# Optimization experiments

Measured on AMD Instinct MI355X. Metric: run time of the kernel, lower is better.

## Reference

```python
import jax, jax.numpy as jnp
import numpy as np

B, N, D_MODEL = 8, 1024, 512
H, DK = 8, 64
STATIONS = 128
MASK_NEG = -1e9
LN_EPS = 1e-6


def setup_inputs() -> dict:
    key = jax.random.key(0)
    ks = jax.random.split(key, 9)
    return {
        "hidden_states": jax.random.normal(ks[0], (B, N, D_MODEL), dtype=jnp.float32),
        "rpe": jax.random.normal(ks[1], (B, H, N, N), dtype=jnp.float32) * 0.1,
        "Wq": jax.random.normal(ks[2], (H * DK, D_MODEL), dtype=jnp.float32) * 0.02,
        "Wk": jax.random.normal(ks[3], (H * DK, D_MODEL), dtype=jnp.float32) * 0.02,
        "Wv": jax.random.normal(ks[4], (H * DK, D_MODEL), dtype=jnp.float32) * 0.02,
        "fc_w": jax.random.normal(ks[5], (D_MODEL, H * DK), dtype=jnp.float32) * 0.02,
        "fc_b": jnp.zeros((D_MODEL,), dtype=jnp.float32),
        "ln_g": jnp.ones((D_MODEL,), dtype=jnp.float32),
        "ln_b": jnp.zeros((D_MODEL,), dtype=jnp.float32),
    }


def _star_mask(n, stations):
    # q_k_mask: query i attends to key j iff j < stations or i == j
    idx = jnp.arange(n)
    return (idx[None, :] < stations) | (idx[:, None] == idx[None, :])  # [n, n] bool


def reference(hidden_states, rpe, Wq, Wk, Wv, fc_w, fc_b, ln_g, ln_b):
    b, n, _ = hidden_states.shape
    residual = hidden_states
    q = (hidden_states @ Wq.T).reshape(b, n, H, DK)
    k = (hidden_states @ Wk.T).reshape(b, n, H, DK)
    v = (hidden_states @ Wv.T).reshape(b, n, H, DK)
    # sparse star+self-loop QK^T with inline RPE add (dense emulation of QKP_mm_tvm)
    scores = jnp.einsum("bihd,bjhd->bhij", q, k) + rpe  # [b,h,n,n]
    mask = _star_mask(n, STATIONS)
    scores = jnp.where(mask[None, None], scores, MASK_NEG)
    scores = scores / jnp.sqrt(jnp.float32(DK))
    attn = jax.nn.softmax(scores, axis=-1)
    # AttnV_mm_tvm: sparse attn-weights times V
    ctx = jnp.einsum("bhij,bjhd->bihd", attn, v).reshape(b, n, H * DK)
    ctx = ctx @ fc_w.T + fc_b + residual
    mu = jnp.mean(ctx, axis=-1, keepdims=True)
    var = jnp.var(ctx, axis=-1, keepdims=True)
    return (ctx - mu) / jnp.sqrt(var + LN_EPS) * ln_g + ln_b
```

## Files before the change

### kernel.cpp

```cpp
#include <hip/hip_runtime.h>
#include <hip/hip_bf16.h>
#include <math.h>

#define B_  8
#define N_  1024
#define DM  512
#define H_  8
#define DK_ 64
#define ST  128

typedef __attribute__((ext_vector_type(8))) short short8;
typedef __attribute__((ext_vector_type(4))) float floatx4;

#define GLD16(gp, lp)                                                          \
    __builtin_amdgcn_global_load_lds(                                          \
        (const __attribute__((address_space(1))) void*)(gp),                   \
        (__attribute__((address_space(3))) void*)(lp), 16, 0, 0)

__device__ __forceinline__ float b2f(short u) {
    union { unsigned int i; float f; } c;
    c.i = ((unsigned int)(unsigned short)u) << 16;
    return c.f;
}
__device__ __forceinline__ unsigned short f2b(float f) {
    __hip_bfloat16 t = __float2bfloat16(f);
    return *(unsigned short*)&t;
}

struct CastArgs {
    const float* src[5];
    unsigned short* dst[5];
};

__global__ __launch_bounds__(256)
void cast_bf16_kernel(CastArgs a)
{
    const int bx = blockIdx.x;
    int j, base;
    if (bx < 2048) { j = 0; base = bx; }
    else { const int r = bx - 2048; j = 1 + (r >> 7); base = r & 127; }
    const float* __restrict__ s = a.src[j];
    unsigned short* __restrict__ d = a.dst[j];
    const int i = (base * 256 + threadIdx.x) * 8;
    float4 x0 = *(const float4*)&s[i];
    float4 x1 = *(const float4*)&s[i + 4];
    ushort4 o0, o1;
    o0.x = f2b(x0.x); o0.y = f2b(x0.y); o0.z = f2b(x0.z); o0.w = f2b(x0.w);
    o1.x = f2b(x1.x); o1.y = f2b(x1.y); o1.z = f2b(x1.z); o1.w = f2b(x1.w);
    *(ushort4*)&d[i] = o0;
    *(ushort4*)&d[i + 4] = o1;
}

__device__ __forceinline__
void gemm_step(const unsigned short* Ac, const unsigned short* Bc,
               int wm, int wn, int mrow, int koff, floatx4 acc[4][4])
{
    short8 af[4], bf[4];
    #pragma unroll
    for (int t = 0; t < 4; ++t) {
        af[t] = *(const short8*)&Ac[(wm * 64 + t * 16 + mrow) * 32 + koff];
        bf[t] = *(const short8*)&Bc[(wn * 64 + t * 16 + mrow) * 32 + koff];
    }
    #pragma unroll
    for (int mt = 0; mt < 4; ++mt)
        #pragma unroll
        for (int nt = 0; nt < 4; ++nt)
            acc[mt][nt] = __builtin_amdgcn_mfma_f32_16x16x32_bf16(
                af[mt], bf[nt], acc[mt][nt], 0, 0, 0);
}

__device__ __forceinline__
void gemm_core(const unsigned short* __restrict__ A,
               const unsigned short* __restrict__ W,
               int m0, int n0, unsigned short* As, unsigned short* Bs,
               floatx4 acc[4][4])
{
    const int tid = threadIdx.x;
    const int lane = tid & 63;
    const int wave = tid >> 6;
    const int wm = wave >> 1, wn = wave & 1;
    const int srow = tid >> 2;
    const int skq  = (tid & 3) * 8;
    const unsigned short* Ag = A + (size_t)(m0 + srow) * 512 + skq;
    const unsigned short* Bg = W + (size_t)(n0 + srow) * 512 + skq;
    const int mrow = lane & 15;
    const int koff = (lane >> 4) * 8;

    unsigned short* A0 = As;        unsigned short* A1 = As + 4096;
    unsigned short* B0 = Bs;        unsigned short* B1 = Bs + 4096;

#define STAGE4(Ad, Bd, off)                                                    \
    do {                                                                       \
        GLD16(Ag + (off),            &(Ad)[tid * 8]);                          \
        GLD16(Ag + 64 * 512 + (off), &(Ad)[2048 + tid * 8]);                   \
        GLD16(Bg + (off),            &(Bd)[tid * 8]);                          \
        GLD16(Bg + 64 * 512 + (off), &(Bd)[2048 + tid * 8]);                   \
    } while (0)

    STAGE4(A0, B0, 0);
    __syncthreads();

    #pragma unroll
    for (int kt = 0; kt < 512; kt += 64) {
        STAGE4(A1, B1, kt + 32);
        gemm_step(A0, B0, wm, wn, mrow, koff, acc);
        __syncthreads();
        if (kt + 64 < 512)
            STAGE4(A0, B0, kt + 64);
        gemm_step(A1, B1, wm, wn, mrow, koff, acc);
        __syncthreads();
    }
#undef STAGE4
}

__global__ __launch_bounds__(256)
void qkv_gemm_kernel(const unsigned short* __restrict__ A,
                     const unsigned short* __restrict__ W0,
                     const unsigned short* __restrict__ W1,
                     const unsigned short* __restrict__ W2,
                     unsigned short* __restrict__ qo,
                     unsigned short* __restrict__ ko,
                     unsigned short* __restrict__ vto)
{
    __shared__ __align__(16) unsigned short As[2 * 128 * 32];
    __shared__ __align__(16) unsigned short Bs[2 * 128 * 32];
    const int by = blockIdx.y;
    const int sel = by >> 2;
    const unsigned short* W = (sel == 0) ? W0 : (sel == 1 ? W1 : W2);
    const int m0 = blockIdx.x * 128;
    const int n0 = (by & 3) * 128;

    floatx4 acc[4][4];
    #pragma unroll
    for (int i = 0; i < 4; ++i)
        #pragma unroll
        for (int j = 0; j < 4; ++j)
            acc[i][j] = (floatx4){0.f, 0.f, 0.f, 0.f};

    gemm_core(A, W, m0, n0, As, Bs, acc);

    const int lane = threadIdx.x & 63;
    const int wave = threadIdx.x >> 6;
    const int wm = wave >> 1, wn = wave & 1;
    const int lx = lane & 15;
    const int rq = (lane >> 4) * 4;

    if (sel == 2) {
        #pragma unroll
        for (int mt = 0; mt < 4; ++mt) {
            const int mrow = m0 + wm * 64 + mt * 16 + rq;
            const int bb = mrow >> 10, tok = mrow & 1023;
            #pragma unroll
            for (int nt = 0; nt < 4; ++nt) {
                const int c = n0 + wn * 64 + nt * 16 + lx;
                const int hh = c >> 6, d = c & 63;
                ushort4 pk;
                pk.x = f2b(acc[mt][nt][0]); pk.y = f2b(acc[mt][nt][1]);
                pk.z = f2b(acc[mt][nt][2]); pk.w = f2b(acc[mt][nt][3]);
                *(ushort4*)&vto[((size_t)(bb * H_ + hh) * DK_ + d) * N_ + tok] = pk;
            }
        }
    } else {
        unsigned short* O = (sel == 0) ? qo : ko;
        #pragma unroll
        for (int mt = 0; mt < 4; ++mt) {
            const int mrow = m0 + wm * 64 + mt * 16 + rq;
            const int bb = mrow >> 10, tok = mrow & 1023;
            #pragma unroll
            for (int nt = 0; nt < 4; ++nt) {
                const int c = n0 + wn * 64 + nt * 16 + lx;
                const int hh = c >> 6, d = c & 63;
                unsigned short* p =
                    O + ((size_t)(bb * H_ + hh) * N_ + tok) * DK_ + d;
                #pragma unroll
                for (int r = 0; r < 4; ++r)
                    p[(size_t)r * DK_] = f2b(acc[mt][nt][r]);
            }
        }
    }
}

__global__ __launch_bounds__(256)
void attn_kernel(const unsigned short* __restrict__ qg,
                 const unsigned short* __restrict__ kg,
                 const unsigned short* __restrict__ vtg,
                 const float* __restrict__ rpe,
                 unsigned short* __restrict__ ctx)
{
    __shared__ __align__(16) unsigned short P[64 * 136];
    __shared__ __align__(16) unsigned short Vd[64 * 72];

    const int tid  = threadIdx.x;
    const int lane = tid & 63;
    const int w    = tid >> 6;
    const int lx   = lane & 15;
    const int quad = lane >> 4;
    const int qb = blockIdx.x * 64;
    const int h  = blockIdx.y, b = blockIdx.z;
    const int bh = b * H_ + h;
    const unsigned short* qh  = qg  + (size_t)bh * N_ * DK_;
    const unsigned short* kh  = kg  + (size_t)bh * N_ * DK_;
    const unsigned short* vth = vtg + (size_t)bh * DK_ * N_;
    const float* rp = rpe + ((size_t)bh * N_ + qb) * N_;
    const bool has_self = (qb >= ST);

    if (has_self) {
        const int d = tid >> 2, t16 = (tid & 3) * 16;
        const unsigned short* vs = vth + (size_t)d * N_ + qb + t16;
        *(short8*)&Vd[d * 72 + t16]     = *(const short8*)vs;
        *(short8*)&Vd[d * 72 + t16 + 8] = *(const short8*)(vs + 8);
    }

    float sself = -1e30f;
    if (has_self) {
        const int i = qb + w * 16 + lx;
        const unsigned short* qr = qh + (size_t)i * DK_ + quad * 16;
        const unsigned short* kr = kh + (size_t)i * DK_ + quad * 16;
        short8 q0 = *(const short8*)qr, q1 = *(const short8*)(qr + 8);
        short8 k0 = *(const short8*)kr, k1 = *(const short8*)(kr + 8);
        float dot = 0.f;
        #pragma unroll
        for (int j = 0; j < 8; ++j) {
            dot = fmaf(b2f(q0[j]), b2f(k0[j]), dot);
            dot = fmaf(b2f(q1[j]), b2f(k1[j]), dot);
        }
        dot += __shfl_xor(dot, 16, 64);
        dot += __shfl_xor(dot, 32, 64);
        const float rd = rp[(size_t)(w * 16 + lx) * N_ + (qb + w * 16 + lx)];
        sself = (dot + rd) * 0.125f;
    }

    float rv[4][8];
    {
        const float* rbase = rp + (size_t)(w * 16 + quad * 4) * N_ + lx;
        #pragma unroll
        for (int r = 0; r < 4; ++r)
            #pragma unroll
            for (int nt = 0; nt < 8; ++nt)
                rv[r][nt] = rbase[(size_t)r * N_ + nt * 16];
    }

    short8 aq[2];
    {
        const unsigned short* qrow =
            qh + (size_t)(qb + w * 16 + lx) * DK_ + quad * 8;
        aq[0] = *(const short8*)qrow;
        aq[1] = *(const short8*)(qrow + 32);
    }
    floatx4 sacc[8];
    #pragma unroll
    for (int nt = 0; nt < 8; ++nt) sacc[nt] = (floatx4){0.f, 0.f, 0.f, 0.f};
    #pragma unroll
    for (int nt = 0; nt < 8; ++nt) {
        const unsigned short* krow =
            kh + (size_t)(nt * 16 + lx) * DK_ + quad * 8;
        short8 b0 = *(const short8*)krow;
        short8 b1 = *(const short8*)(krow + 32);
        sacc[nt] = __builtin_amdgcn_mfma_f32_16x16x32_bf16(aq[0], b0, sacc[nt], 0, 0, 0);
        sacc[nt] = __builtin_amdgcn_mfma_f32_16x16x32_bf16(aq[1], b1, sacc[nt], 0, 0, 0);
    }

    float l4[4], ps4[4];
    #pragma unroll
    for (int r = 0; r < 4; ++r) {
        float sv[8];
        float mx = -1e30f;
        #pragma unroll
        for (int nt = 0; nt < 8; ++nt) {
            sv[nt] = (sacc[nt][r] + rv[r][nt]) * 0.125f;
            mx = fmaxf(mx, sv[nt]);
        }
        #pragma unroll
        for (int o = 1; o < 16; o <<= 1)
            mx = fmaxf(mx, __shfl_xor(mx, o, 64));
        const float ss = __shfl(sself, quad * 4 + r, 64);
        mx = fmaxf(mx, ss);
        float sum = 0.f;
        #pragma unroll
        for (int nt = 0; nt < 8; ++nt) {
            sv[nt] = __expf(sv[nt] - mx);
            sum += sv[nt];
        }
// ... 157 lines not shown
                s[mt][r]  += __shfl_xor(s[mt][r],  o, 64);
                ss[mt][r] += __shfl_xor(ss[mt][r], o, 64);
            }
    if (lx == 0) {
        #pragma unroll
        for (int mt = 0; mt < 2; ++mt)
            #pragma unroll
            for (int r = 0; r < 4; ++r) {
                lsum[mt * 16 + quad * 4 + r][wv] = s[mt][r];
                lsq [mt * 16 + quad * 4 + r][wv] = ss[mt][r];
            }
    }
    __syncthreads();

    #pragma unroll
    for (int mt = 0; mt < 2; ++mt)
        #pragma unroll
        for (int r = 0; r < 4; ++r) {
            const int rl = mt * 16 + quad * 4 + r;
            float ts = 0.f, tss = 0.f;
            #pragma unroll
            for (int u = 0; u < 8; ++u) { ts += lsum[rl][u]; tss += lsq[rl][u]; }
            const float mean = ts * (1.0f / DM);
            const float var  = tss * (1.0f / DM) - mean * mean;
            const float rstd = rsqrtf(var + 1e-6f);
            const size_t row = (size_t)(m0 + rl);
            #pragma unroll
            for (int nt = 0; nt < 4; ++nt) {
                const int c = wv * 64 + nt * 16 + lx;
                out[row * 512 + c] =
                    (acc[mt][nt][r] - mean) * rstd * g[c] + bb[c];
            }
        }
}

extern "C" void kernel_launch(void* const* d_in, const int* in_sizes, int n_in,
                              void* d_out, int out_size, void* d_ws, size_t ws_size,
                              hipStream_t stream)
{
    (void)in_sizes; (void)n_in; (void)out_size; (void)ws_size;
    const float* hidden = (const float*)d_in[0];
    const float* rpe    = (const float*)d_in[1];
    const float* Wq     = (const float*)d_in[2];
    const float* Wk     = (const float*)d_in[3];
    const float* Wv     = (const float*)d_in[4];
    const float* fc_w   = (const float*)d_in[5];
    const float* fc_b   = (const float*)d_in[6];
    const float* ln_g   = (const float*)d_in[7];
    const float* ln_b   = (const float*)d_in[8];
    float* out = (float*)d_out;
    char* ws = (char*)d_ws;

    const size_t MB = 1024 * 1024;
    unsigned short* hb  = (unsigned short*)(ws + 0 * MB);
    unsigned short* wq  = (unsigned short*)(ws + 8 * MB);
    unsigned short* wk  = (unsigned short*)(ws + 8 * MB + 512 * 1024);
    unsigned short* wv  = (unsigned short*)(ws + 9 * MB);
    unsigned short* wf  = (unsigned short*)(ws + 9 * MB + 512 * 1024);
    unsigned short* qB  = (unsigned short*)(ws + 16 * MB);
    unsigned short* kB  = (unsigned short*)(ws + 24 * MB);
    unsigned short* vtB = (unsigned short*)(ws + 32 * MB);
    unsigned short* cb  = (unsigned short*)(ws + 40 * MB);

    CastArgs ca;
    ca.src[0] = hidden; ca.dst[0] = hb;
    ca.src[1] = Wq;     ca.dst[1] = wq;
    ca.src[2] = Wk;     ca.dst[2] = wk;
    ca.src[3] = Wv;     ca.dst[3] = wv;
    ca.src[4] = fc_w;   ca.dst[4] = wf;
    cast_bf16_kernel<<<dim3(2048 + 4 * 128), 256, 0, stream>>>(ca);

    qkv_gemm_kernel<<<dim3(64, 12), 256, 0, stream>>>(hb, wq, wk, wv, qB, kB, vtB);
    attn_kernel<<<dim3(16, H_, B_), 256, 0, stream>>>(qB, kB, vtB, rpe, cb);
    fc_ln_kernel<<<dim3(256), 512, 0, stream>>>(cb, wf, fc_b, hidden, ln_g, ln_b, out);
}
```

Measured before the change: 390.2 us.

## Fuse Q and K projections, precompute self-dot, store only station keys

The QKV GEMM now computes Q and K in the same block from a shared A tile. In the epilogue it computes each token's q·k self-loop dot product and writes it to a float buffer. Only the first 128 station keys are written to global memory, which removes most of the K store traffic and the per-token K reload in the attention kernel. The attention kernel reads the precomputed self-dot instead of recomputing it. In exchange, the M tile shrinks to 64, the grid changes to 128x8, and the Q/K blocks carry more accumulators and LDS, which may reduce occupancy.

Measured after the change: 392.6 us. About the same (+0.6%).

```diff
diff --git a/kernel.cpp b/kernel.cpp
--- a/kernel.cpp
+++ b/kernel.cpp
@@ -51,68 +51,6 @@
     *(ushort4*)&d[i + 4] = o1;
 }
 
-__device__ __forceinline__
-void gemm_step(const unsigned short* Ac, const unsigned short* Bc,
-               int wm, int wn, int mrow, int koff, floatx4 acc[4][4])
-{
-    short8 af[4], bf[4];
-    #pragma unroll
-    for (int t = 0; t < 4; ++t) {
-        af[t] = *(const short8*)&Ac[(wm * 64 + t * 16 + mrow) * 32 + koff];
-        bf[t] = *(const short8*)&Bc[(wn * 64 + t * 16 + mrow) * 32 + koff];
-    }
-    #pragma unroll
-    for (int mt = 0; mt < 4; ++mt)
-        #pragma unroll
-        for (int nt = 0; nt < 4; ++nt)
-            acc[mt][nt] = __builtin_amdgcn_mfma_f32_16x16x32_bf16(
-                af[mt], bf[nt], acc[mt][nt], 0, 0, 0);
-}
-
-__device__ __forceinline__
-void gemm_core(const unsigned short* __restrict__ A,
-               const unsigned short* __restrict__ W,
-               int m0, int n0, unsigned short* As, unsigned short* Bs,
-               floatx4 acc[4][4])
-{
-    const int tid = threadIdx.x;
-    const int lane = tid & 63;
-    const int wave = tid >> 6;
-    const int wm = wave >> 1, wn = wave & 1;
-    const int srow = tid >> 2;
-    const int skq  = (tid & 3) * 8;
-    const unsigned short* Ag = A + (size_t)(m0 + srow) * 512 + skq;
-    const unsigned short* Bg = W + (size_t)(n0 + srow) * 512 + skq;
-    const int mrow = lane & 15;
-    const int koff = (lane >> 4) * 8;
-
-    unsigned short* A0 = As;        unsigned short* A1 = As + 4096;
-    unsigned short* B0 = Bs;        unsigned short* B1 = Bs + 4096;
-
-#define STAGE4(Ad, Bd, off)                                                    \
-    do {                                                                       \
-        GLD16(Ag + (off),            &(Ad)[tid * 8]);                          \
-        GLD16(Ag + 64 * 512 + (off), &(Ad)[2048 + tid * 8]);                   \
-        GLD16(Bg + (off),            &(Bd)[tid * 8]);                          \
-        GLD16(Bg + 64 * 512 + (off), &(Bd)[2048 + tid * 8]);                   \
-    } while (0)
-
-    STAGE4(A0, B0, 0);
-    __syncthreads();
-
-    #pragma unroll
-    for (int kt = 0; kt < 512; kt += 64) {
-        STAGE4(A1, B1, kt + 32);
-        gemm_step(A0, B0, wm, wn, mrow, koff, acc);
-        __syncthreads();
-        if (kt + 64 < 512)
-            STAGE4(A0, B0, kt + 64);
-        gemm_step(A1, B1, wm, wn, mrow, koff, acc);
-        __syncthreads();
-    }
-#undef STAGE4
-}
-
 __global__ __launch_bounds__(256)
 void qkv_gemm_kernel(const unsigned short* __restrict__ A,
                      const unsigned short* __restrict__ W0,
@@ -120,61 +58,200 @@
                      const unsigned short* __restrict__ W2,
                      unsigned short* __restrict__ qo,
                      unsigned short* __restrict__ ko,
-                     unsigned short* __restrict__ vto)
+                     unsigned short* __restrict__ vto,
+                     float* __restrict__ sdot)
 {
-    __shared__ __align__(16) unsigned short As[2 * 128 * 32];
+    __shared__ __align__(16) unsigned short As[2 * 64 * 32];
     __shared__ __align__(16) unsigned short Bs[2 * 128 * 32];
+    __shared__ __align__(16) unsigned short Cs[2 * 128 * 32];
+
+    const int tid  = threadIdx.x;
+    const int lane = tid & 63;
+    const int wave = tid >> 6;
+    const int wm = wave >> 1, wn = wave & 1;
     const int by = blockIdx.y;
-    const int sel = by >> 2;
-    const unsigned short* W = (sel == 0) ? W0 : (sel == 1 ? W1 : W2);
-    const int m0 = blockIdx.x * 128;
+    const int qk = (by < 4);
     const int n0 = (by & 3) * 128;
-
-    floatx4 acc[4][4];
-    #pragma unroll
-    for (int i = 0; i < 4; ++i)
-        #pragma unroll
-        for (int j = 0; j < 4; ++j)
-            acc[i][j] = (floatx4){0.f, 0.f, 0.f, 0.f};
-
-    gemm_core(A, W, m0, n0, As, Bs, acc);
-
-    const int lane = threadIdx.x & 63;
-    const int wave = threadIdx.x >> 6;
-    const int wm = wave >> 1, wn = wave & 1;
-    const int lx = lane & 15;
-    const int rq = (lane >> 4) * 4;
-
-    if (sel == 2) {
-        #pragma unroll
-        for (int mt = 0; mt < 4; ++mt) {
-            const int mrow = m0 + wm * 64 + mt * 16 + rq;
-            const int bb = mrow >> 10, tok = mrow & 1023;
+    const int m0 = blockIdx.x * 64;
+
+    const int srow = tid >> 2;
+    const int skq  = (tid & 3) * 8;
+    const unsigned short* Ag  = A  + (size_t)(m0 + srow) * 512 + skq;
+    const unsigned short* Bqg = (qk ? W0 : W2) + (size_t)(n0 + srow) * 512 + skq;
+    const unsigned short* Bkg = W1 + (size_t)(n0 + srow) * 512 + skq;
+
+    const int mrow = lane & 15;
+    const int koff = (lane >> 4) * 8;
+    const int lx   = lane & 15;
+    const int quad = lane >> 4;
+    const int rq   = quad * 4;
+
+    unsigned short* A0 = As;  unsigned short* A1 = As + 2048;
+    unsigned short* B0 = Bs;  unsigned short* B1 = Bs + 4096;
+    unsigned short* C0 = Cs;  unsigned short* C1 = Cs + 4096;
+
+    if (qk) {
+        floatx4 aq[2][4], ak[2][4];
+        #pragma unroll
+        for (int i = 0; i < 2; ++i)
+            #pragma unroll
+            for (int j = 0; j < 4; ++j) {
+                aq[i][j] = (floatx4){0.f, 0.f, 0.f, 0.f};
+                ak[i][j] = (floatx4){0.f, 0.f, 0.f, 0.f};
+            }
+
+#define STAGE_QK(Ad, Bd, Cd, off)                                              \
+    do {                                                                       \
+        GLD16(Ag + (off),            &(Ad)[tid * 8]);                          \
+        GLD16(Bqg + (off),           &(Bd)[tid * 8]);                          \
+        GLD16(Bqg + 64 * 512 + (off), &(Bd)[2048 + tid * 8]);                  \
+        GLD16(Bkg + (off),           &(Cd)[tid * 8]);                          \
+        GLD16(Bkg + 64 * 512 + (off), &(Cd)[2048 + tid * 8]);                  \
+    } while (0)
+
+#define STEP_QK(Ad, Bd, Cd)                                                    \
+    do {                                                                       \
+        short8 af[2], bq[4], bk[4];                                            \
+        _Pragma("unroll")                                                      \
+        for (int t = 0; t < 2; ++t)                                            \
+            af[t] = *(const short8*)&(Ad)[(wm * 32 + t * 16 + mrow) * 32 + koff];\
+        _Pragma("unroll")                                                      \
+        for (int t = 0; t < 4; ++t) {                                          \
+            bq[t] = *(const short8*)&(Bd)[(wn * 64 + t * 16 + mrow) * 32 + koff];\
+            bk[t] = *(const short8*)&(Cd)[(wn * 64 + t * 16 + mrow) * 32 + koff];\
+        }                                                                      \
+        _Pragma("unroll")                                                      \
+        for (int mt = 0; mt < 2; ++mt)                                         \
+            _Pragma("unroll")                                                  \
+            for (int nt = 0; nt < 4; ++nt) {                                   \
+                aq[mt][nt] = __builtin_amdgcn_mfma_f32_16x16x32_bf16(          \
+                    af[mt], bq[nt], aq[mt][nt], 0, 0, 0);                      \
+                ak[mt][nt] = __builtin_amdgcn_mfma_f32_16x16x32_bf16(          \
+                    af[mt], bk[nt], ak[mt][nt], 0, 0, 0);                      \
+            }                                                                  \
+    } while (0)
+
+        STAGE_QK(A0, B0, C0, 0);
+        __syncthreads();
+        #pragma unroll
+        for (int kt = 0; kt < 512; kt += 64) {
+            STAGE_QK(A1, B1, C1, kt + 32);
+            STEP_QK(A0, B0, C0);
+            __syncthreads();
+            if (kt + 64 < 512)
+                STAGE_QK(A0, B0, C0, kt + 64);
+            STEP_QK(A1, B1, C1);
+            __syncthreads();
+        }
+#undef STAGE_QK
+#undef STEP_QK
+
+        const int hh = (n0 >> 6) + wn;
+        #pragma unroll
+        for (int mt = 0; mt < 2; ++mt) {
+            const int mr = m0 + wm * 32 + mt * 16 + rq;
+            const int bb = mr >> 10, tok = mr & 1023;
+            #pragma unroll
+            for (int nt = 0; nt < 4; ++nt) {
+                const int d = nt * 16 + lx;
+                unsigned short* p =
+                    qo + ((size_t)(bb * H_ + hh) * N_ + tok) * DK_ + d;
+                #pragma unroll
+                for (int r = 0; r < 4; ++r)
+                    p[(size_t)r * DK_] = f2b(aq[mt][nt][r]);
+            }
+        }
+        #pragma unroll
+        for (int mt = 0; mt < 2; ++mt)
+            #pragma unroll
+            for (int r = 0; r < 4; ++r) {
+                float dp = 0.f;
+                #pragma unroll
+                for (int nt = 0; nt < 4; ++nt)
+                    dp = fmaf(aq[mt][nt][r], ak[mt][nt][r], dp);
+                #pragma unroll
+                for (int o = 1; o < 16; o <<= 1)
+                    dp += __shfl_xor(dp, o, 64);
+                if (lx == 0) {
+                    const int mr = m0 + wm * 32 + mt * 16 + rq + r;
+                    sdot[((size_t)((mr >> 10) * H_ + hh)) * N_ + (mr & 1023)] = dp;
+                }
+            }
+        if ((m0 & 1023) < ST) {
+            #pragma unroll
+            for (int mt = 0; mt < 2; ++mt) {
+                const int mr = m0 + wm * 32 + mt * 16 + rq;
+                const int bb = mr >> 10, tok = mr & 1023;
+                #pragma unroll
+                for (int nt = 0; nt < 4; ++nt) {
+                    const int d = nt * 16 + lx;
+                    unsigned short* p =
+                        ko + ((size_t)(bb * H_ + hh) * ST + tok) * DK_ + d;
+                    #pragma unroll
+                    for (int r = 0; r < 4; ++r)
+                        p[(size_t)r * DK_] = f2b(ak[mt][nt][r]);
+                }
+            }
+        }
+    } else {
+        floatx4 av[2][4];
+        #pragma unroll
+        for (int i = 0; i < 2; ++i)
+            #pragma unroll
+            for (int j = 0; j < 4; ++j)
+                av[i][j] = (floatx4){0.f, 0.f, 0.f, 0.f};
+
+#define STAGE_V(Ad, Bd, off)                                                   \
+    do {                                                                       \
+        GLD16(Ag + (off),             &(Ad)[tid * 8]);                         \
+        GLD16(Bqg + (off),            &(Bd)[tid * 8]);                         \
+        GLD16(Bqg + 64 * 512 + (off), &(Bd)[2048 + tid * 8]);                  \
+    } while (0)
+
+#define STEP_V(Ad, Bd)                                                         \
+    do {                                                                       \
+        short8 af[2], bv[4];                                                   \
+        _Pragma("unroll")                                                      \
+        for (int t = 0; t < 2; ++t)                                            \
+            af[t] = *(const short8*)&(Ad)[(wm * 32 + t * 16 + mrow) * 32 + koff];\
+        _Pragma("unroll")                                                      \
+        for (int t = 0; t < 4; ++t)                                            \
+            bv[t] = *(const short8*)&(Bd)[(wn * 64 + t * 16 + mrow) * 32 + koff];\
+        _Pragma("unroll")                                                      \
+        for (int mt = 0; mt < 2; ++mt)                                         \
+            _Pragma("unroll")                                                  \
+            for (int nt = 0; nt < 4; ++nt)                                     \
+                av[mt][nt] = __builtin_amdgcn_mfma_f32_16x16x32_bf16(          \
+                    af[mt], bv[nt], av[mt][nt], 0, 0, 0);                      \
+    } while (0)
+
+        STAGE_V(A0, B0, 0);
+        __syncthreads();
+        #pragma unroll
+        for (int kt = 0; kt < 512; kt += 64) {
+            STAGE_V(A1, B1, kt + 32);
+            STEP_V(A0, B0);
+            __syncthreads();
+            if (kt + 64 < 512)
+                STAGE_V(A0, B0, kt + 64);
+            STEP_V(A1, B1);
+            __syncthreads();
+        }
+#undef STAGE_V
+#undef STEP_V
+
+        #pragma unroll
+        for (int mt = 0; mt < 2; ++mt) {
+            const int mr = m0 + wm * 32 + mt * 16 + rq;
+            const int bb = mr >> 10, tok = mr & 1023;
             #pragma unroll
             for (int nt = 0; nt < 4; ++nt) {
                 const int c = n0 + wn * 64 + nt * 16 + lx;
                 const int hh = c >> 6, d = c & 63;
                 ushort4 pk;
-                pk.x = f2b(acc[mt][nt][0]); pk.y = f2b(acc[mt][nt][1]);
-                pk.z = f2b(acc[mt][nt][2]); pk.w = f2b(acc[mt][nt][3]);
+                pk.x = f2b(av[mt][nt][0]); pk.y = f2b(av[mt][nt][1]);
+                pk.z = f2b(av[mt][nt][2]); pk.w = f2b(av[mt][nt][3]);
                 *(ushort4*)&vto[((size_t)(bb * H_ + hh) * DK_ + d) * N_ + tok] = pk;
-            }
-        }
-    } else {
-        unsigned short* O = (sel == 0) ? qo : ko;
-        #pragma unroll
-        for (int mt = 0; mt < 4; ++mt) {
-            const int mrow = m0 + wm * 64 + mt * 16 + rq;
-            const int bb = mrow >> 10, tok = mrow & 1023;
-            #pragma unroll
-            for (int nt = 0; nt < 4; ++nt) {
-                const int c = n0 + wn * 64 + nt * 16 + lx;
-                const int hh = c >> 6, d = c & 63;
-                unsigned short* p =
-                    O + ((size_t)(bb * H_ + hh) * N_ + tok) * DK_ + d;
-                #pragma unroll
-                for (int r = 0; r < 4; ++r)
-                    p[(size_t)r * DK_] = f2b(acc[mt][nt][r]);
             }
         }
     }
@@ -185,6 +262,7 @@
                  const unsigned short* __restrict__ kg,
                  const unsigned short* __restrict__ vtg,
                  const float* __restrict__ rpe,
+                 const float* __restrict__ sdotp,
                  unsigned short* __restrict__ ctx)
 {
     __shared__ __align__(16) unsigned short P[64 * 136];
@@ -199,7 +277,7 @@
     const int h  = blockIdx.y, b = blockIdx.z;
     const int bh = b * H_ + h;
     const unsigned short* qh  = qg  + (size_t)bh * N_ * DK_;
-    const unsigned short* kh  = kg  + (size_t)bh * N_ * DK_;
+    const unsigned short* kh  = kg  + (size_t)bh * ST * DK_;
     const unsigned short* vth = vtg + (size_t)bh * DK_ * N_;
     const float* rp = rpe + ((size_t)bh * N_ + qb) * N_;
     const bool has_self = (qb >= ST);
@@ -214,20 +292,9 @@
     float sself = -1e30f;
     if (has_self) {
         const int i = qb + w * 16 + lx;
-        const unsigned short* qr = qh + (size_t)i * DK_ + quad * 16;
-        const unsigned short* kr = kh + (size_t)i * DK_ + quad * 16;
-        short8 q0 = *(const short8*)qr, q1 = *(const short8*)(qr + 8);
-        short8 k0 = *(const short8*)kr, k1 = *(const short8*)(kr + 8);
-        float dot = 0.f;
-        #pragma unroll
-        for (int j = 0; j < 8; ++j) {
-            dot = fmaf(b2f(q0[j]), b2f(k0[j]), dot);
-            dot = fmaf(b2f(q1[j]), b2f(k1[j]), dot);
-        }
-        dot += __shfl_xor(dot, 16, 64);
-        dot += __shfl_xor(dot, 32, 64);
-        const float rd = rp[(size_t)(w * 16 + lx) * N_ + (qb + w * 16 + lx)];
-        sself = (dot + rd) * 0.125f;
+        const float sd = sdotp[(size_t)bh * N_ + i];
+        const float rd = rp[(size_t)(w * 16 + lx) * N_ + i];
+        sself = (sd + rd) * 0.125f;
     }
 
     float rv[4][8];
@@ -498,6 +565,7 @@
     unsigned short* wf  = (unsigned short*)(ws + 9 * MB + 512 * 1024);
     unsigned short* qB  = (unsigned short*)(ws + 16 * MB);
     unsigned short* kB  = (unsigned short*)(ws + 24 * MB);
+    float*          sd  = (float*)(ws + 25 * MB);
     unsigned short* vtB = (unsigned short*)(ws + 32 * MB);
     unsigned short* cb  = (unsigned short*)(ws + 40 * MB);
 
@@ -509,7 +577,8 @@
     ca.src[4] = fc_w;   ca.dst[4] = wf;
     cast_bf16_kernel<<<dim3(2048 + 4 * 128), 256, 0, stream>>>(ca);
 
-    qkv_gemm_kernel<<<dim3(64, 12), 256, 0, stream>>>(hb, wq, wk, wv, qB, kB, vtB);
-    attn_kernel<<<dim3(16, H_, B_), 256, 0, stream>>>(qB, kB, vtB, rpe, cb);
+    qkv_gemm_kernel<<<dim3(128, 8), 256, 0, stream>>>(hb, wq, wk, wv,
+                                                      qB, kB, vtB, sd);
+    attn_kernel<<<dim3(16, H_, B_), 256, 0, stream>>>(qB, kB, vtB, rpe, sd, cb);
     fc_ln_kernel<<<dim3(256), 512, 0, stream>>>(cb, wf, fc_b, hidden, ln_g, ln_b, out);
 }
```

## Fuse all four stages into one persistent cooperative kernel with grid syncs

Applied to the files above, without the earlier changes.

Replaces the four separate launches (cast, QKV GEMM, attention, FC+LayerNorm) with a single cooperative kernel of 256 blocks x 512 threads. Each stage runs as a loop over work items and stages are separated by grid.sync. The aim is to remove launch gaps and inter-kernel tail effects. In exchange each stage runs with a fixed 256-block grid and 512-thread blocks, which may lower occupancy or parallelism compared with the original per-stage grids, and grid barriers add their own cost. If the cooperative launch fails, the original four-kernel path runs instead.

Result: slower. 650.8 us (+66.8%).

```diff
diff --git a/kernel.cpp b/kernel.cpp
--- a/kernel.cpp
+++ b/kernel.cpp
@@ -1,6 +1,9 @@
 #include <hip/hip_runtime.h>
 #include <hip/hip_bf16.h>
+#include <hip/hip_cooperative_groups.h>
 #include <math.h>
+
+namespace cg = cooperative_groups;
 
 #define B_  8
 #define N_  1024
@@ -25,6 +28,453 @@
 __device__ __forceinline__ unsigned short f2b(float f) {
     __hip_bfloat16 t = __float2bfloat16(f);
     return *(unsigned short*)&t;
+}
+
+struct FusedArgs {
+    const float* hidden;
+    const float* rpe;
+    const float* Wq;
+    const float* Wk;
+    const float* Wv;
+    const float* fc_w;
+    const float* fc_b;
+    const float* ln_g;
+    const float* ln_b;
+    float* out;
+    unsigned short* hb;
+    unsigned short* wq;
+    unsigned short* wk;
+    unsigned short* wv;
+    unsigned short* wf;
+    unsigned short* qB;
+    unsigned short* kB;
+    unsigned short* vtB;
+    unsigned short* cb;
+};
+
+#define SMEM_BYTES 71680
+
+__global__ __launch_bounds__(512, 2)
+void fused_all(FusedArgs a)
+{
+    __shared__ __align__(16) unsigned char smem[SMEM_BYTES];
+    cg::grid_group grid = cg::this_grid();
+
+    const int tid  = threadIdx.x;
+    const int bid  = blockIdx.x;
+    const int lane = tid & 63;
+    const int wave = tid >> 6;
+    const int lx   = lane & 15;
+    const int quad = lane >> 4;
+    const int mrow = lx;
+    const int koff = quad * 8;
+
+    {
+        const float* wsrc[4] = { a.Wq, a.Wk, a.Wv, a.fc_w };
+        unsigned short* wdst[4] = { a.wq, a.wk, a.wv, a.wf };
+        const int gid = bid * 512 + tid;
+        #pragma unroll
+        for (int it = 0; it < 5; ++it) {
+            const int idx = it * 131072 + gid;
+            const float* s;
+            unsigned short* d;
+            int off;
+            if (idx < 524288) { s = a.hidden; d = a.hb; off = idx; }
+            else {
+                const int r2 = idx - 524288;
+                const int sl = r2 >> 15;
+                s = wsrc[sl]; d = wdst[sl]; off = r2 & 32767;
+            }
+            const int i = off * 8;
+            float4 x0 = *(const float4*)&s[i];
+            float4 x1 = *(const float4*)&s[i + 4];
+            ushort4 o0, o1;
+            o0.x = f2b(x0.x); o0.y = f2b(x0.y); o0.z = f2b(x0.z); o0.w = f2b(x0.w);
+            o1.x = f2b(x1.x); o1.y = f2b(x1.y); o1.z = f2b(x1.z); o1.w = f2b(x1.w);
+            *(ushort4*)&d[i] = o0;
+            *(ushort4*)&d[i + 4] = o1;
+        }
+    }
+    __threadfence();
+    grid.sync();
+
+    {
+        unsigned short* As = (unsigned short*)smem;
+        unsigned short* Bs = As + 8192;
+        unsigned short* A0 = As;  unsigned short* A1 = As + 4096;
+        unsigned short* B0 = Bs;  unsigned short* B1 = Bs + 4096;
+        const int wm = wave >> 2;
+        const int wn = wave & 3;
+        const int srow = tid >> 2;
+        const int skq  = (tid & 3) * 8;
+        const int rq   = quad * 4;
+
+        for (int t = 0; t < 3; ++t) {
+            const int jid = t * 256 + bid;
+            const int by  = jid >> 6;
+            const int sel = by >> 2;
+            const int n0  = (by & 3) * 128;
+            const int m0  = (jid & 63) * 128;
+            const unsigned short* W =
+                (sel == 0) ? a.wq : (sel == 1 ? a.wk : a.wv);
+            const unsigned short* Ag = a.hb + (size_t)(m0 + srow) * 512 + skq;
+            const unsigned short* Bg = W + (size_t)(n0 + srow) * 512 + skq;
+
+            floatx4 acc[4][2];
+            #pragma unroll
+            for (int i = 0; i < 4; ++i)
+                #pragma unroll
+                for (int j = 0; j < 2; ++j)
+                    acc[i][j] = (floatx4){0.f, 0.f, 0.f, 0.f};
+
+#define QSTAGE(Ad, Bd, off)                                                    \
+    do {                                                                       \
+        GLD16(Ag + (off), &(Ad)[tid * 8]);                                     \
+        GLD16(Bg + (off), &(Bd)[tid * 8]);                                     \
+    } while (0)
+#define QSTEP(Ad, Bd)                                                          \
+    do {                                                                       \
+        short8 af[4], bf[2];                                                   \
+        _Pragma("unroll")                                                      \
+        for (int tt = 0; tt < 4; ++tt)                                         \
+            af[tt] = *(const short8*)&(Ad)[(wm * 64 + tt * 16 + mrow) * 32 + koff];\
+        _Pragma("unroll")                                                      \
+        for (int tt = 0; tt < 2; ++tt)                                         \
+            bf[tt] = *(const short8*)&(Bd)[(wn * 32 + tt * 16 + mrow) * 32 + koff];\
+        _Pragma("unroll")                                                      \
+        for (int mt = 0; mt < 4; ++mt)                                         \
+            _Pragma("unroll")                                                  \
+            for (int nt = 0; nt < 2; ++nt)                                     \
+                acc[mt][nt] = __builtin_amdgcn_mfma_f32_16x16x32_bf16(         \
+                    af[mt], bf[nt], acc[mt][nt], 0, 0, 0);                     \
+    } while (0)
+
+            QSTAGE(A0, B0, 0);
+            __syncthreads();
+            #pragma unroll
+            for (int kt = 0; kt < 512; kt += 64) {
+                QSTAGE(A1, B1, kt + 32);
+                QSTEP(A0, B0);
+                __syncthreads();
+                if (kt + 64 < 512)
+                    QSTAGE(A0, B0, kt + 64);
+                QSTEP(A1, B1);
+                __syncthreads();
+            }
+#undef QSTAGE
+#undef QSTEP
+
+            if (sel == 2) {
+                #pragma unroll
+                for (int mt = 0; mt < 4; ++mt) {
+                    const int mr = m0 + wm * 64 + mt * 16 + rq;
+                    const int bb = mr >> 10, tok = mr & 1023;
+                    #pragma unroll
+                    for (int nt = 0; nt < 2; ++nt) {
+                        const int c = n0 + wn * 32 + nt * 16 + lx;
+                        const int hh = c >> 6, d = c & 63;
+                        ushort4 pk;
+                        pk.x = f2b(acc[mt][nt][0]); pk.y = f2b(acc[mt][nt][1]);
+                        pk.z = f2b(acc[mt][nt][2]); pk.w = f2b(acc[mt][nt][3]);
+                        *(ushort4*)&a.vtB[((size_t)(bb * H_ + hh) * DK_ + d) * N_ + tok] = pk;
+                    }
+                }
+            } else {
+                unsigned short* O = (sel == 0) ? a.qB : a.kB;
+                #pragma unroll
+                for (int mt = 0; mt < 4; ++mt) {
+                    const int mr = m0 + wm * 64 + mt * 16 + rq;
+                    const int bb = mr >> 10, tok = mr & 1023;
+                    #pragma unroll
+                    for (int nt = 0; nt < 2; ++nt) {
+                        const int c = n0 + wn * 32 + nt * 16 + lx;
+                        const int hh = c >> 6, d = c & 63;
+                        unsigned short* p =
+                            O + ((size_t)(bb * H_ + hh) * N_ + tok) * DK_ + d;
+                        #pragma unroll
+                        for (int r = 0; r < 4; ++r)
+                            p[(size_t)r * DK_] = f2b(acc[mt][nt][r]);
+                    }
+                }
+            }
+            __syncthreads();
+        }
+    }
+    __threadfence();
+    grid.sync();
+
+    {
+        unsigned short* P  = (unsigned short*)smem;
+        unsigned short* Vd = P + 128 * 136;
+        const int w = wave;
+
+        for (int jj = 0; jj < 2; ++jj) {
+            const int jid = jj * 256 + bid;
+            const int qb  = (jid & 7) * 128;
+            const int bh  = jid >> 3;
+            const int h   = bh & 7, b = bh >> 3;
+            const unsigned short* qh  = a.qB  + (size_t)bh * N_ * DK_;
+            const unsigned short* kh  = a.kB  + (size_t)bh * N_ * DK_;
+            const unsigned short* vth = a.vtB + (size_t)bh * DK_ * N_;
+            const float* rp = a.rpe + ((size_t)bh * N_ + qb) * N_;
+            const bool has_self = (qb >= ST);
+
+            __syncthreads();
+
+            if (has_self) {
+                const int d = tid >> 3, t16 = (tid & 7) * 16;
+                const unsigned short* vs = vth + (size_t)d * N_ + qb + t16;
+                *(short8*)&Vd[d * 136 + t16]     = *(const short8*)vs;
+                *(short8*)&Vd[d * 136 + t16 + 8] = *(const short8*)(vs + 8);
+            }
+
+            float sself = -1e30f;
+            if (has_self) {
+                const int i = qb + w * 16 + lx;
+                const unsigned short* qr = qh + (size_t)i * DK_ + quad * 16;
+                const unsigned short* kr = kh + (size_t)i * DK_ + quad * 16;
+                short8 q0 = *(const short8*)qr, q1 = *(const short8*)(qr + 8);
+                short8 k0 = *(const short8*)kr, k1 = *(const short8*)(kr + 8);
+                float dot = 0.f;
+                #pragma unroll
+                for (int j = 0; j < 8; ++j) {
+                    dot = fmaf(b2f(q0[j]), b2f(k0[j]), dot);
+                    dot = fmaf(b2f(q1[j]), b2f(k1[j]), dot);
+                }
+                dot += __shfl_xor(dot, 16, 64);
+                dot += __shfl_xor(dot, 32, 64);
+                const float rd = rp[(size_t)(w * 16 + lx) * N_ + i];
+                sself = (dot + rd) * 0.125f;
+            }
+
+            float rv[4][8];
+            {
+                const float* rbase = rp + (size_t)(w * 16 + quad * 4) * N_ + lx;
+                #pragma unroll
+                for (int r = 0; r < 4; ++r)
+                    #pragma unroll
+                    for (int nt = 0; nt < 8; ++nt)
+                        rv[r][nt] = rbase[(size_t)r * N_ + nt * 16];
+            }
+
+            short8 aq[2];
+            {
+                const unsigned short* qrow =
+                    qh + (size_t)(qb + w * 16 + lx) * DK_ + quad * 8;
+                aq[0] = *(const short8*)qrow;
+                aq[1] = *(const short8*)(qrow + 32);
+            }
+            floatx4 sacc[8];
+            #pragma unroll
+            for (int nt = 0; nt < 8; ++nt) sacc[nt] = (floatx4){0.f, 0.f, 0.f, 0.f};
+            #pragma unroll
+            for (int nt = 0; nt < 8; ++nt) {
+                const unsigned short* krow =
+                    kh + (size_t)(nt * 16 + lx) * DK_ + quad * 8;
+                short8 b0 = *(const short8*)krow;
+                short8 b1 = *(const short8*)(krow + 32);
+                sacc[nt] = __builtin_amdgcn_mfma_f32_16x16x32_bf16(aq[0], b0, sacc[nt], 0, 0, 0);
+                sacc[nt] = __builtin_amdgcn_mfma_f32_16x16x32_bf16(aq[1], b1, sacc[nt], 0, 0, 0);
+            }
+
+            float l4[4], ps4[4];
+            #pragma unroll
+            for (int r = 0; r < 4; ++r) {
+                float sv[8];
+                float mx = -1e30f;
+                #pragma unroll
+                for (int nt = 0; nt < 8; ++nt) {
+                    sv[nt] = (sacc[nt][r] + rv[r][nt]) * 0.125f;
+                    mx = fmaxf(mx, sv[nt]);
+                }
+                #pragma unroll
+                for (int o = 1; o < 16; o <<= 1)
+                    mx = fmaxf(mx, __shfl_xor(mx, o, 64));
+                const float ss = __shfl(sself, quad * 4 + r, 64);
+                mx = fmaxf(mx, ss);
+                float sum = 0.f;
+                #pragma unroll
+                for (int nt = 0; nt < 8; ++nt) {
+                    sv[nt] = __expf(sv[nt] - mx);
+                    sum += sv[nt];
+                }
+                #pragma unroll
+                for (int o = 1; o < 16; o <<= 1)
+                    sum += __shfl_xor(sum, o, 64);
+                const float ps = has_self ? __expf(ss - mx) : 0.f;
+                l4[r] = sum + ps;
+                ps4[r] = ps;
+                const int row = w * 16 + quad * 4 + r;
+                #pragma unroll
+                for (int nt = 0; nt < 8; ++nt)
+                    P[row * 136 + nt * 16 + lx] = f2b(sv[nt]);
+            }
+            __syncthreads();
+
+            short8 ap[4];
+            #pragma unroll
+            for (int ks = 0; ks < 4; ++ks)
+                ap[ks] = *(const short8*)&P[(w * 16 + lx) * 136 + ks * 32 + quad * 8];
+            floatx4 oacc[4];
+            #pragma unroll
+            for (int nt = 0; nt < 4; ++nt) oacc[nt] = (floatx4){0.f, 0.f, 0.f, 0.f};
+            #pragma unroll
+            for (int nt = 0; nt < 4; ++nt) {
+                const unsigned short* vrow = vth + (size_t)(nt * 16 + lx) * N_;
+                #pragma unroll
+                for (int ks = 0; ks < 4; ++ks) {
+                    short8 bv = *(const short8*)(vrow + ks * 32 + quad * 8);
+                    oacc[nt] = __builtin_amdgcn_mfma_f32_16x16x32_bf16(ap[ks], bv, oacc[nt], 0, 0, 0);
+                }
+            }
+
+            #pragma unroll
+            for (int r = 0; r < 4; ++r) {
+                const int il = w * 16 + quad * 4 + r;
+                const int i = qb + il;
+                const float inv = 1.0f / l4[r];
+                const float ps = ps4[r];
+                #pragma unroll
+                for (int nt = 0; nt < 4; ++nt) {
+                    const int d = nt * 16 + lx;
+                    float o = oacc[nt][r];
+                    if (has_self)
+                        o = fmaf(ps, b2f((short)Vd[d * 136 + il]), o);
+                    a.cb[((size_t)(b * N_) + i) * DM + h * DK_ + d] = f2b(o * inv);
+                }
+            }
+            __syncthreads();
+        }
+    }
+    __threadfence();
+    grid.sync();
+
+    {
+        unsigned short* As = (unsigned short*)smem;
+        unsigned short* Bs = As + 2048;
+        float* lsum = (float*)(smem + 69632);
+        float* lsq  = (float*)(smem + 70656);
+        unsigned short* A0 = As;  unsigned short* A1 = As + 1024;
+        unsigned short* B0 = Bs;  unsigned short* B1 = Bs + 16384;
+
+        const int wv   = wave;
+        const int m0   = bid * 32;
+        const int srow = tid >> 2;
+        const int skq  = (tid & 3) * 8;
+        const unsigned short* Ag = a.cb + (size_t)(m0 + srow) * 512 + skq;
+        const unsigned short* Bg = a.wf + (size_t)srow * 512 + skq;
+
+#define FSTAGE(Ad, Bd, off)                                                    \
+    do {                                                                       \
+        if (tid < 128) GLD16(Ag + (off), &(Ad)[tid * 8]);                      \
+        _Pragma("unroll")                                                      \
+        for (int p = 0; p < 4; ++p)                                            \
+            GLD16(Bg + (size_t)p * 128 * 512 + (off),                          \
+                  &(Bd)[p * 4096 + tid * 8]);                                  \
+    } while (0)
+#define FSTEP(Ad, Bd)                                                          \
+    do {                                                                       \
+        short8 af[2], bf[4];                                                   \
+        _Pragma("unroll")                                                      \
+        for (int tt = 0; tt < 2; ++tt)                                         \
+            af[tt] = *(const short8*)&(Ad)[(tt * 16 + mrow) * 32 + koff];      \
+        _Pragma("unroll")                                                      \
+        for (int tt = 0; tt < 4; ++tt)                                         \
+            bf[tt] = *(const short8*)&(Bd)[(wv * 64 + tt * 16 + mrow) * 32 + koff];\
+        _Pragma("unroll")                                                      \
+        for (int mt = 0; mt < 2; ++mt)                                         \
+            _Pragma("unroll")                                                  \
+            for (int nt = 0; nt < 4; ++nt)                                     \
+                acc[mt][nt] = __builtin_amdgcn_mfma_f32_16x16x32_bf16(         \
+                    af[mt], bf[nt], acc[mt][nt], 0, 0, 0);                     \
+    } while (0)
+
+        floatx4 acc[2][4];
+        #pragma unroll
+        for (int i = 0; i < 2; ++i)
+            #pragma unroll
+            for (int j = 0; j < 4; ++j)
+                acc[i][j] = (floatx4){0.f, 0.f, 0.f, 0.f};
+
+        FSTAGE(A0, B0, 0);
+        __syncthreads();
+        #pragma unroll
+        for (int kt = 0; kt < 512; kt += 64) {
+            FSTAGE(A1, B1, kt + 32);
+            FSTEP(A0, B0);
+            __syncthreads();
+            if (kt + 64 < 512)
+                FSTAGE(A0, B0, kt + 64);
+            FSTEP(A1, B1);
+            __syncthreads();
+        }
+#undef FSTAGE
+#undef FSTEP
+
+        float s[2][4], ss[2][4];
+        #pragma unroll
+        for (int mt = 0; mt < 2; ++mt)
+            #pragma unroll
+            for (int r = 0; r < 4; ++r) { s[mt][r] = 0.f; ss[mt][r] = 0.f; }
+
+        #pragma unroll
+        for (int mt = 0; mt < 2; ++mt)
+            #pragma unroll
+            for (int nt = 0; nt < 4; ++nt) {
+                const int c = wv * 64 + nt * 16 + lx;
+                const float bvv = a.fc_b[c];
+                #pragma unroll
+                for (int r = 0; r < 4; ++r) {
+                    const size_t row = (size_t)(m0 + mt * 16 + quad * 4 + r);
+                    float v = acc[mt][nt][r] + bvv + a.hidden[row * 512 + c];
+                    acc[mt][nt][r] = v;
+                    s[mt][r] += v;
+                    ss[mt][r] = fmaf(v, v, ss[mt][r]);
+                }
+            }
+
+        #pragma unroll
+        for (int o = 1; o < 16; o <<= 1)
+            #pragma unroll
+            for (int mt = 0; mt < 2; ++mt)
+                #pragma unroll
+                for (int r = 0; r < 4; ++r) {
+                    s[mt][r]  += __shfl_xor(s[mt][r],  o, 64);
+                    ss[mt][r] += __shfl_xor(ss[mt][r], o, 64);
+                }
+        if (lx == 0) {
+            #pragma unroll
+            for (int mt = 0; mt < 2; ++mt)
+                #pragma unroll
+                for (int r = 0; r < 4; ++r) {
+                    lsum[(mt * 16 + quad * 4 + r) * 8 + wv] = s[mt][r];
+                    lsq [(mt * 16 + quad * 4 + r) * 8 + wv] = ss[mt][r];
+                }
+        }
+        __syncthreads();
+
+        #pragma unroll
+        for (int mt = 0; mt < 2; ++mt)
+            #pragma unroll
+            for (int r = 0; r < 4; ++r) {
+                const int rl = mt * 16 + quad * 4 + r;
+                float ts = 0.f, tss = 0.f;
+                #pragma unroll
+                for (int u = 0; u < 8; ++u) {
+                    ts += lsum[rl * 8 + u]; tss += lsq[rl * 8 + u];
+                }
+                const float mean = ts * (1.0f / DM);
+                const float var  = tss * (1.0f / DM) - mean * mean;
+                const float rstd = rsqrtf(var + 1e-6f);
+                const size_t row = (size_t)(m0 + rl);
+                #pragma unroll
+                for (int nt = 0; nt < 4; ++nt) {
+                    const int c = wv * 64 + nt * 16 + lx;
+                    a.out[row * 512 + c] =
+                        (acc[mt][nt][r] - mean) * rstd * a.ln_g[c] + a.ln_b[c];
+                }
+            }
+    }
 }
 
 struct CastArgs {
@@ -226,7 +676,7 @@
         }
         dot += __shfl_xor(dot, 16, 64);
         dot += __shfl_xor(dot, 32, 64);
-        const float rd = rp[(size_t)(w * 16 + lx) * N_ + (qb + w * 16 + lx)];
+        const float rd = rp[(size_t)(w * 16 + lx) * N_ + i];
         sself = (dot + rd) * 0.125f;
     }
 
@@ -501,15 +951,29 @@
     unsigned short* vtB = (unsigned short*)(ws + 32 * MB);
     unsigned short* cb  = (unsigned short*)(ws + 40 * MB);
 
-    CastArgs ca;
-    ca.src[0] = hidden; ca.dst[0] = hb;
-    ca.src[1] = Wq;     ca.dst[1] = wq;
-    ca.src[2] = Wk;     ca.dst[2] = wk;
-    ca.src[3] = Wv;     ca.dst[3] = wv;
-    ca.src[4] = fc_w;   ca.dst[4] = wf;
-    cast_bf16_kernel<<<dim3(2048 + 4 * 128), 256, 0, stream>>>(ca);
-
-    qkv_gemm_kernel<<<dim3(64, 12), 256, 0, stream>>>(hb, wq, wk, wv, qB, kB, vtB);
-    attn_kernel<<<dim3(16, H_, B_), 256, 0, stream>>>(qB, kB, vtB, rpe, cb);
-    fc_ln_kernel<<<dim3(256), 512, 0, stream>>>(cb, wf, fc_b, hidden, ln_g, ln_b, out);
-}
+    FusedArgs fa;
+    fa.hidden = hidden; fa.rpe = rpe;
+    fa.Wq = Wq; fa.Wk = Wk; fa.Wv = Wv; fa.fc_w = fc_w; fa.fc_b = fc_b;
+    fa.ln_g = ln_g; fa.ln_b = ln_b; fa.out = out;
+    fa.hb = hb; fa.wq = wq; fa.wk = wk; fa.wv = wv; fa.wf = wf;
+    fa.qB = qB; fa.kB = kB; fa.vtB = vtB; fa.cb = cb;
+
+    void* kargs[] = { (void*)&fa };
+    hipError_t e = hipLaunchCooperativeKernel(
+        (const void*)fused_all, dim3(256), dim3(512), kargs, 0, stream);
+
+    if (e != hipSuccess) {
+        CastArgs ca;
+        ca.src[0] = hidden; ca.dst[0] = hb;
+        ca.src[1] = Wq;     ca.dst[1] = wq;
+        ca.src[2] = Wk;     ca.dst[2] = wk;
+        ca.src[3] = Wv;     ca.dst[3] = wv;
+        ca.src[4] = fc_w;   ca.dst[4] = wf;
+        cast_bf16_kernel<<<dim3(2048 + 4 * 128), 256, 0, stream>>>(ca);
+        qkv_gemm_kernel<<<dim3(64, 12), 256, 0, stream>>>(hb, wq, wk, wv,
+                                                          qB, kB, vtB);
+        attn_kernel<<<dim3(16, H_, B_), 256, 0, stream>>>(qB, kB, vtB, rpe, cb);
+        fc_ln_kernel<<<dim3(256), 512, 0, stream>>>(cb, wf, fc_b, hidden,
+                                                    ln_g, ln_b, out);
+    }
+}
```

## Fuse fp32-to-bf16 casts into QKV GEMM and attention kernels

Applied to the files above, without the earlier changes.

Removes the standalone cast kernel. The QKV GEMM now loads fp32 activations and weights directly, converts them to bf16 in registers and stores them into single-buffered LDS, with register prefetch of the next K slice. The fc_w cast moves into a subset of attention blocks. This saves a launch and an extra read/write round-trip of the bf16 copies. In exchange the GEMM reads twice the global bytes, loses its async global-to-LDS double buffering and adds two barriers per K step.

New measurement: 403.8 us. 3.5% more time.

```diff
diff --git a/kernel.cpp b/kernel.cpp
--- a/kernel.cpp
+++ b/kernel.cpp
@@ -26,110 +26,45 @@
     __hip_bfloat16 t = __float2bfloat16(f);
     return *(unsigned short*)&t;
 }
-
-struct CastArgs {
-    const float* src[5];
-    unsigned short* dst[5];
-};
+__device__ __forceinline__ short8 cvt8(float4 x0, float4 x1) {
+    short8 r;
+    r[0] = (short)f2b(x0.x); r[1] = (short)f2b(x0.y);
+    r[2] = (short)f2b(x0.z); r[3] = (short)f2b(x0.w);
+    r[4] = (short)f2b(x1.x); r[5] = (short)f2b(x1.y);
+    r[6] = (short)f2b(x1.z); r[7] = (short)f2b(x1.w);
+    return r;
+}
 
 __global__ __launch_bounds__(256)
-void cast_bf16_kernel(CastArgs a)
-{
-    const int bx = blockIdx.x;
-    int j, base;
-    if (bx < 2048) { j = 0; base = bx; }
-    else { const int r = bx - 2048; j = 1 + (r >> 7); base = r & 127; }
-    const float* __restrict__ s = a.src[j];
-    unsigned short* __restrict__ d = a.dst[j];
-    const int i = (base * 256 + threadIdx.x) * 8;
-    float4 x0 = *(const float4*)&s[i];
-    float4 x1 = *(const float4*)&s[i + 4];
-    ushort4 o0, o1;
-    o0.x = f2b(x0.x); o0.y = f2b(x0.y); o0.z = f2b(x0.z); o0.w = f2b(x0.w);
-    o1.x = f2b(x1.x); o1.y = f2b(x1.y); o1.z = f2b(x1.z); o1.w = f2b(x1.w);
-    *(ushort4*)&d[i] = o0;
-    *(ushort4*)&d[i + 4] = o1;
-}
-
-__device__ __forceinline__
-void gemm_step(const unsigned short* Ac, const unsigned short* Bc,
-               int wm, int wn, int mrow, int koff, floatx4 acc[4][4])
-{
-    short8 af[4], bf[4];
-    #pragma unroll
-    for (int t = 0; t < 4; ++t) {
-        af[t] = *(const short8*)&Ac[(wm * 64 + t * 16 + mrow) * 32 + koff];
-        bf[t] = *(const short8*)&Bc[(wn * 64 + t * 16 + mrow) * 32 + koff];
-    }
-    #pragma unroll
-    for (int mt = 0; mt < 4; ++mt)
-        #pragma unroll
-        for (int nt = 0; nt < 4; ++nt)
-            acc[mt][nt] = __builtin_amdgcn_mfma_f32_16x16x32_bf16(
-                af[mt], bf[nt], acc[mt][nt], 0, 0, 0);
-}
-
-__device__ __forceinline__
-void gemm_core(const unsigned short* __restrict__ A,
-               const unsigned short* __restrict__ W,
-               int m0, int n0, unsigned short* As, unsigned short* Bs,
-               floatx4 acc[4][4])
-{
-    const int tid = threadIdx.x;
-    const int lane = tid & 63;
-    const int wave = tid >> 6;
-    const int wm = wave >> 1, wn = wave & 1;
-    const int srow = tid >> 2;
-    const int skq  = (tid & 3) * 8;
-    const unsigned short* Ag = A + (size_t)(m0 + srow) * 512 + skq;
-    const unsigned short* Bg = W + (size_t)(n0 + srow) * 512 + skq;
-    const int mrow = lane & 15;
-    const int koff = (lane >> 4) * 8;
-
-    unsigned short* A0 = As;        unsigned short* A1 = As + 4096;
-    unsigned short* B0 = Bs;        unsigned short* B1 = Bs + 4096;
-
-#define STAGE4(Ad, Bd, off)                                                    \
-    do {                                                                       \
-        GLD16(Ag + (off),            &(Ad)[tid * 8]);                          \
-        GLD16(Ag + 64 * 512 + (off), &(Ad)[2048 + tid * 8]);                   \
-        GLD16(Bg + (off),            &(Bd)[tid * 8]);                          \
-        GLD16(Bg + 64 * 512 + (off), &(Bd)[2048 + tid * 8]);                   \
-    } while (0)
-
-    STAGE4(A0, B0, 0);
-    __syncthreads();
-
-    #pragma unroll
-    for (int kt = 0; kt < 512; kt += 64) {
-        STAGE4(A1, B1, kt + 32);
-        gemm_step(A0, B0, wm, wn, mrow, koff, acc);
-        __syncthreads();
-        if (kt + 64 < 512)
-            STAGE4(A0, B0, kt + 64);
-        gemm_step(A1, B1, wm, wn, mrow, koff, acc);
-        __syncthreads();
-    }
-#undef STAGE4
-}
-
-__global__ __launch_bounds__(256)
-void qkv_gemm_kernel(const unsigned short* __restrict__ A,
-                     const unsigned short* __restrict__ W0,
-                     const unsigned short* __restrict__ W1,
-                     const unsigned short* __restrict__ W2,
+void qkv_gemm_kernel(const float* __restrict__ A32,
+                     const float* __restrict__ W0,
+                     const float* __restrict__ W1,
+                     const float* __restrict__ W2,
                      unsigned short* __restrict__ qo,
                      unsigned short* __restrict__ ko,
                      unsigned short* __restrict__ vto)
 {
-    __shared__ __align__(16) unsigned short As[2 * 128 * 32];
-    __shared__ __align__(16) unsigned short Bs[2 * 128 * 32];
+    __shared__ __align__(16) unsigned short As[128 * 32];
+    __shared__ __align__(16) unsigned short Bs[128 * 32];
+
+    const int tid  = threadIdx.x;
+    const int lane = tid & 63;
+    const int wave = tid >> 6;
+    const int wm = wave >> 1, wn = wave & 1;
     const int by = blockIdx.y;
     const int sel = by >> 2;
-    const unsigned short* W = (sel == 0) ? W0 : (sel == 1 ? W1 : W2);
+    const float* W = (sel == 0) ? W0 : (sel == 1 ? W1 : W2);
     const int m0 = blockIdx.x * 128;
     const int n0 = (by & 3) * 128;
 
+    const int srow = tid >> 2;
+    const int skq  = (tid & 3) * 8;
+    const float* Ag = A32 + (size_t)(m0 + srow) * 512 + skq;
+    const float* Bg = W   + (size_t)(n0 + srow) * 512 + skq;
+    const int mrow = lane & 15;
+    const int koff = (lane >> 4) * 8;
+    const int ldso = srow * 32 + skq;
+
     floatx4 acc[4][4];
     #pragma unroll
     for (int i = 0; i < 4; ++i)
@@ -137,19 +72,52 @@
         for (int j = 0; j < 4; ++j)
             acc[i][j] = (floatx4){0.f, 0.f, 0.f, 0.f};
 
-    gemm_core(A, W, m0, n0, As, Bs, acc);
-
-    const int lane = threadIdx.x & 63;
-    const int wave = threadIdx.x >> 6;
-    const int wm = wave >> 1, wn = wave & 1;
+    float4 a0, a1, a2, a3, b0, b1, b2, b3;
+#define LOADS(off)                                                             \
+    do {                                                                       \
+        a0 = *(const float4*)(Ag + (off));                                     \
+        a1 = *(const float4*)(Ag + (off) + 4);                                 \
+        a2 = *(const float4*)(Ag + 64 * 512 + (off));                          \
+        a3 = *(const float4*)(Ag + 64 * 512 + (off) + 4);                      \
+        b0 = *(const float4*)(Bg + (off));                                     \
+        b1 = *(const float4*)(Bg + (off) + 4);                                 \
+        b2 = *(const float4*)(Bg + 64 * 512 + (off));                          \
+        b3 = *(const float4*)(Bg + 64 * 512 + (off) + 4);                      \
+    } while (0)
+
+    LOADS(0);
+    for (int kt = 0; kt < 512; kt += 32) {
+        __syncthreads();
+        *(short8*)&As[ldso]        = cvt8(a0, a1);
+        *(short8*)&As[2048 + ldso] = cvt8(a2, a3);
+        *(short8*)&Bs[ldso]        = cvt8(b0, b1);
+        *(short8*)&Bs[2048 + ldso] = cvt8(b2, b3);
+        __syncthreads();
+        if (kt + 32 < 512)
+            LOADS(kt + 32);
+        short8 af[4], bf[4];
+        #pragma unroll
+        for (int t = 0; t < 4; ++t) {
+            af[t] = *(const short8*)&As[(wm * 64 + t * 16 + mrow) * 32 + koff];
+            bf[t] = *(const short8*)&Bs[(wn * 64 + t * 16 + mrow) * 32 + koff];
+        }
+        #pragma unroll
+        for (int mt = 0; mt < 4; ++mt)
+            #pragma unroll
+            for (int nt = 0; nt < 4; ++nt)
+                acc[mt][nt] = __builtin_amdgcn_mfma_f32_16x16x32_bf16(
+                    af[mt], bf[nt], acc[mt][nt], 0, 0, 0);
+    }
+#undef LOADS
+
     const int lx = lane & 15;
     const int rq = (lane >> 4) * 4;
 
     if (sel == 2) {
         #pragma unroll
         for (int mt = 0; mt < 4; ++mt) {
-            const int mrow = m0 + wm * 64 + mt * 16 + rq;
-            const int bb = mrow >> 10, tok = mrow & 1023;
+            const int mr = m0 + wm * 64 + mt * 16 + rq;
+            const int bb = mr >> 10, tok = mr & 1023;
             #pragma unroll
             for (int nt = 0; nt < 4; ++nt) {
                 const int c = n0 + wn * 64 + nt * 16 + lx;
@@ -164,8 +132,8 @@
         unsigned short* O = (sel == 0) ? qo : ko;
         #pragma unroll
         for (int mt = 0; mt < 4; ++mt) {
-            const int mrow = m0 + wm * 64 + mt * 16 + rq;
-            const int bb = mrow >> 10, tok = mrow & 1023;
+            const int mr = m0 + wm * 64 + mt * 16 + rq;
+            const int bb = mr >> 10, tok = mr & 1023;
             #pragma unroll
             for (int nt = 0; nt < 4; ++nt) {
                 const int c = n0 + wn * 64 + nt * 16 + lx;
@@ -185,12 +153,26 @@
                  const unsigned short* __restrict__ kg,
                  const unsigned short* __restrict__ vtg,
                  const float* __restrict__ rpe,
+                 const float* __restrict__ fcw,
+                 unsigned short* __restrict__ wf,
                  unsigned short* __restrict__ ctx)
 {
     __shared__ __align__(16) unsigned short P[64 * 136];
     __shared__ __align__(16) unsigned short Vd[64 * 72];
 
     const int tid  = threadIdx.x;
+
+    if (blockIdx.z == 0 && blockIdx.y == 0) {
+        const int base = blockIdx.x * 256 + tid;
+        #pragma unroll
+        for (int it = 0; it < 8; ++it) {
+            const int i = (it * 4096 + base) * 8;
+            float4 x0 = *(const float4*)&fcw[i];
+            float4 x1 = *(const float4*)&fcw[i + 4];
+            *(short8*)&wf[i] = cvt8(x0, x1);
+        }
+    }
+
     const int lane = tid & 63;
     const int w    = tid >> 6;
     const int lx   = lane & 15;
@@ -491,25 +473,16 @@
     char* ws = (char*)d_ws;
 
     const size_t MB = 1024 * 1024;
-    unsigned short* hb  = (unsigned short*)(ws + 0 * MB);
-    unsigned short* wq  = (unsigned short*)(ws + 8 * MB);
-    unsigned short* wk  = (unsigned short*)(ws + 8 * MB + 512 * 1024);
-    unsigned short* wv  = (unsigned short*)(ws + 9 * MB);
     unsigned short* wf  = (unsigned short*)(ws + 9 * MB + 512 * 1024);
     unsigned short* qB  = (unsigned short*)(ws + 16 * MB);
     unsigned short* kB  = (unsigned short*)(ws + 24 * MB);
     unsigned short* vtB = (unsigned short*)(ws + 32 * MB);
     unsigned short* cb  = (unsigned short*)(ws + 40 * MB);
 
-    CastArgs ca;
-    ca.src[0] = hidden; ca.dst[0] = hb;
-    ca.src[1] = Wq;     ca.dst[1] = wq;
-    ca.src[2] = Wk;     ca.dst[2] = wk;
-    ca.src[3] = Wv;     ca.dst[3] = wv;
-    ca.src[4] = fc_w;   ca.dst[4] = wf;
-    cast_bf16_kernel<<<dim3(2048 + 4 * 128), 256, 0, stream>>>(ca);
-
-    qkv_gemm_kernel<<<dim3(64, 12), 256, 0, stream>>>(hb, wq, wk, wv, qB, kB, vtB);
-    attn_kernel<<<dim3(16, H_, B_), 256, 0, stream>>>(qB, kB, vtB, rpe, cb);
-    fc_ln_kernel<<<dim3(256), 512, 0, stream>>>(cb, wf, fc_b, hidden, ln_g, ln_b, out);
-}
+    qkv_gemm_kernel<<<dim3(64, 12), 256, 0, stream>>>(hidden, Wq, Wk, Wv,
+                                                      qB, kB, vtB);
+    attn_kernel<<<dim3(16, H_, B_), 256, 0, stream>>>(qB, kB, vtB, rpe,
+                                                      fc_w, wf, cb);
+    fc_ln_kernel<<<dim3(256), 512, 0, stream>>>(cb, wf, fc_b, hidden,
+                                                ln_g, ln_b, out);
+}
```
